# Kernel tuning notes

Hardware: AMD Instinct MI355X
Metric: run time of the kernel (lower is better)

The kernel has to match this reference:

```python
import jax, jax.numpy as jnp
import numpy as np
from jax import lax

B, S, H, A = 8, 2048, 16, 128   # batch, seq, num_head, i_head_dim
D = 128                          # o_head_dim
LN_EPS = 1e-6


def setup_inputs() -> dict:
    key = jax.random.key(0)
    ks = jax.random.split(key, 6)
    heads_input = jax.random.normal(ks[0], (B, S, H, A), dtype=jnp.float32)
    # grouped linear weights: (heads, in_per_head, out_per_head)
    w_hid = jax.random.normal(ks[1], (H, 2 * A, 3 * D), dtype=jnp.float32) * 0.02
    b_hid = jnp.zeros((H, 3 * D), dtype=jnp.float32)
    w_og = jax.random.normal(ks[2], (H, A + D, D), dtype=jnp.float32) * 0.02
    b_og = jnp.zeros((H, D), dtype=jnp.float32)
    ln_g = jnp.ones((H, A), dtype=jnp.float32)
    ln_b = jnp.zeros((H, A), dtype=jnp.float32)
    init_cx = jnp.zeros((H, D), dtype=jnp.float32)
    return {"heads_input": heads_input, "w_hid": w_hid, "b_hid": b_hid,
            "w_og": w_og, "b_og": b_og, "ln_g": ln_g, "ln_b": ln_b,
            "init_cx": init_cx}


def _ln2d(x, g, b):
    # LayerNorm over the last two dims (H, A)
    m = jnp.mean(x, axis=(-2, -1), keepdims=True)
    v = jnp.var(x, axis=(-2, -1), keepdims=True)
    return (x - m) * lax.rsqrt(v + LN_EPS) * g + b


def _forward(heads_input, w_hid, b_hid, w_og, b_og, ln_g, ln_b, init_cx):
    # cumulative-sum + LayerNorm (RS1cumsumstatnorm, states=None)
    csum = _ln2d(jnp.cumsum(heads_input, axis=1), ln_g, ln_b)  # (B,S,H,A)
    # grouped (per-head) linear: 2A -> 3D
    hid_in = jnp.concatenate([heads_input, csum], axis=-1)     # (B,S,H,2A)
    gates = jnp.einsum('bshi,hio->bsho', hid_in, w_hid) + b_hid  # (B,S,H,3D)
    igate, fgate, hidden = jnp.split(gates, 3, axis=-1)
    fgate = jax.nn.sigmoid(fgate)
    hidden = jax.nn.relu(hidden)
    igh = jax.nn.sigmoid(igate) * hidden                        # (B,S,H,D)
    # forget-gated linear recurrence c_t = f_t * c_{t-1} + igh_t (LGateFunc)
    def combine(c1, c2):
        a1, u1 = c1
        a2, u2 = c2
        return a1 * a2, u1 * a2 + u2
    F, C = lax.associative_scan(combine, (fgate, igh), axis=1)
    cell = C + F * init_cx[None, None]                          # (B,S,H,D)
    # output gate: grouped linear (A+D -> D), sigmoid, gate the cell
    og_in = jnp.concatenate([heads_input, cell], axis=-1)       # (B,S,H,A+D)
    og = jax.nn.sigmoid(jnp.einsum('bshi,hio->bsho', og_in, w_og) + b_og)
    return og * cell


def reference(heads_input, w_hid, b_hid, w_og, b_og, ln_g, ln_b, init_cx):
    return _forward(heads_input, w_hid, b_hid, w_og, b_og, ln_g, ln_b, init_cx)
```

## Files before the change

### kernel.cpp

```cpp
#include <hip/hip_runtime.h>
#include <stdint.h>

#define Bb 8
#define Ss 2048
#define Hh 16
#define Aa 128
#define Dd 128
#define NGATE 384
#define KDIM 256
#define NCH 16
#define CLEN 128
#define ROWS (Bb*Ss)
#define ROWSTR (Hh*Aa)

typedef float f32x4 __attribute__((ext_vector_type(4)));
typedef __bf16 bf16x8 __attribute__((ext_vector_type(8)));
typedef unsigned short u16x8 __attribute__((ext_vector_type(8)));

static __device__ __forceinline__ unsigned short f2bf(float f){
  unsigned int u = __builtin_bit_cast(unsigned int, f);
  u += 0x7FFFu + ((u >> 16) & 1u);
  return (unsigned short)(u >> 16);
}
static __device__ __forceinline__ float bf2f(unsigned short s){
  unsigned int u = ((unsigned int)s) << 16;
  return __builtin_bit_cast(float, u);
}
static __device__ __forceinline__ float sigf(float x){ return 1.0f/(1.0f + __expf(-x)); }

__global__ void k_conv_whid(const float* __restrict__ w, unsigned short* __restrict__ wt){
  int idx = blockIdx.x*256 + threadIdx.x;
  const int total = Hh*KDIM*NGATE;
  for (; idx < total; idx += gridDim.x*256){
    int o = idx % NGATE; int k = (idx/NGATE) % KDIM; int h = idx/(NGATE*KDIM);
    int g = o >> 7, d = o & 127;
    int nh = d >> 6, dl = d & 63;
    int wn = dl >> 4, ln15 = d & 15;
    int ks = k >> 5, lq = (k >> 3) & 3, kb = k & 7;
    int hy = h*2 + nh;
    int l = lq*16 + ln15;
    size_t dst = (size_t)hy*(192*KDIM) + (size_t)((((wn*8 + ks)*3 + g)*64 + l)*8 + kb);
    wt[dst] = f2bf(w[idx]);
  }
}
__global__ void k_conv_wog(const float* __restrict__ w, unsigned short* __restrict__ wt){
  int idx = blockIdx.x*256 + threadIdx.x;
  const int total = Hh*KDIM*Dd;
  for (; idx < total; idx += gridDim.x*256){
    int o = idx % Dd; int k = (idx/Dd) % KDIM; int h = idx/(Dd*KDIM);
    int wn = o >> 5, j = (o >> 4) & 1, ln15 = o & 15;
    int ks = k >> 5, lq = (k >> 3) & 3, kb = k & 7;
    int lane = lq*16 + ln15;
    size_t dst = (size_t)h*(Dd*KDIM) + (size_t)((((wn*8 + ks)*2 + j)*64 + lane)*8 + kb);
    wt[dst] = f2bf(w[idx]);
  }
}

__global__ void k_cumsum_a(const float* __restrict__ x, float* __restrict__ totals,
                           unsigned short* __restrict__ xbf){
  int c = blockIdx.x;
  int k = c % NCH; int hb = c / NCH;
  int b = hb / Hh, h = hb % Hh;
  int a = threadIdx.x;
  const size_t base = ((size_t)(b*Ss + k*CLEN)*Hh + h)*Aa + a;
  const float* p = x + base;
  unsigned short* xq = xbf + base;
  float run = 0.f;
  #pragma unroll 2
  for (int i = 0; i < CLEN; ++i){
    float v = p[(size_t)i*ROWSTR];
    run += v;
    xq[(size_t)i*ROWSTR] = f2bf(v);
  }
  totals[(size_t)c*Aa + a] = run;
}

__global__ void k_cumsum_c(const unsigned short* __restrict__ xbf, const float* __restrict__ totals,
                           unsigned short* __restrict__ csum){
  int c = blockIdx.x;
  int k = c % NCH; int hb = c / NCH;
  int b = hb / Hh, h = hb % Hh;
  int a = threadIdx.x;
  const float* tp = totals + (size_t)hb*NCH*Aa + a;
  float run = 0.f;
  for (int j = 0; j < k; ++j) run += tp[(size_t)j*Aa];
  const size_t base = ((size_t)(b*Ss + k*CLEN)*Hh + h)*Aa + a;
  const unsigned short* p = xbf + base;
  unsigned short* q = csum + base;
  #pragma unroll 2
  for (int i = 0; i < CLEN; ++i){
    run += bf2f(p[(size_t)i*ROWSTR]);
    q[(size_t)i*ROWSTR] = f2bf(run);
  }
}

__global__ void k_stats_ln(unsigned short* __restrict__ cs,
                           const float* __restrict__ ln_g, const float* __restrict__ ln_b){
  int r = blockIdx.x;
  int t = threadIdx.x;
  unsigned short* p = cs + (size_t)r*ROWSTR + t*8;
  u16x8 v = *(const u16x8*)p;
  float s = 0.f, q = 0.f;
  #pragma unroll
  for (int i = 0; i < 8; ++i){ float f = bf2f(v[i]); s += f; q += f*f; }
  #pragma unroll
  for (int off = 32; off; off >>= 1){ s += __shfl_down(s, off); q += __shfl_down(q, off); }
  __shared__ float ls[4], lq[4];
  __shared__ float2 mrs;
  int wid = t >> 6, lane = t & 63;
  if (lane == 0){ ls[wid] = s; lq[wid] = q; }
  __syncthreads();
  if (t == 0){
    float S2 = ls[0]+ls[1]+ls[2]+ls[3], Q = lq[0]+lq[1]+lq[2]+lq[3];
    float mu = S2 * (1.0f/(float)ROWSTR);
    float var = Q * (1.0f/(float)ROWSTR) - mu*mu;
    mrs = make_float2(mu, rsqrtf(var + 1e-6f));
  }
  __syncthreads();
  float mu = mrs.x, rstd = mrs.y;
  const float4* g4 = (const float4*)(ln_g + t*8);
  const float4* b4 = (const float4*)(ln_b + t*8);
  float4 g0 = g4[0], g1 = g4[1], b0 = b4[0], b1 = b4[1];
  u16x8 o;
  o[0] = f2bf((bf2f(v[0]) - mu)*rstd*g0.x + b0.x);
  o[1] = f2bf((bf2f(v[1]) - mu)*rstd*g0.y + b0.y);
  o[2] = f2bf((bf2f(v[2]) - mu)*rstd*g0.z + b0.z);
  o[3] = f2bf((bf2f(v[3]) - mu)*rstd*g0.w + b0.w);
  o[4] = f2bf((bf2f(v[4]) - mu)*rstd*g1.x + b1.x);
  o[5] = f2bf((bf2f(v[5]) - mu)*rstd*g1.y + b1.y);
  o[6] = f2bf((bf2f(v[6]) - mu)*rstd*g1.z + b1.z);
  o[7] = f2bf((bf2f(v[7]) - mu)*rstd*g1.w + b1.w);
  *(u16x8*)p = o;
}

#define GROWT(t_) ((mg*16 + (t_))*128)
__launch_bounds__(512, 2)
__global__ void k_gates(const unsigned short* __restrict__ xbf,
                        const unsigned short* __restrict__ csln,
                        const unsigned short* __restrict__ wht,
                        const float* __restrict__ b_hid, unsigned int* __restrict__ fu){
  __shared__ unsigned short lA[4][128*64];
  const int mg = blockIdx.x, hy = blockIdx.y;
  const int h = hy >> 1, nh = hy & 1;
  const int tid = threadIdx.x;
  const int lane = tid & 63, wid = tid >> 6;
  const int wm = wid & 1, wn = wid >> 1;
  const int ln15 = lane & 15, lq = lane >> 4;
  const int r0 = tid >> 3, q0 = tid & 7;
  const int lwA0 = (r0*128 + q0*16) ^ ((r0 & 7) << 4);
  const int lwA1 = ((r0+64)*128 + q0*16) ^ ((r0 & 7) << 4);

  bf16x8 Bf[8][3];
  {
    const u16x8* bs8 = (const u16x8*)(wht + (size_t)hy*(192*KDIM));
    #pragma unroll
    for (int ks = 0; ks < 8; ++ks)
      #pragma unroll
      for (int g = 0; g < 3; ++g)
        Bf[ks][g] = __builtin_bit_cast(bf16x8, bs8[((wn*8 + ks)*3 + g)*64 + lane]);
  }
  const int dcol = nh*64 + wn*16 + ln15;
  const float big = b_hid[h*NGATE + dcol];
  const float bfg = b_hid[h*NGATE + 128 + dcol];
  const float bhd = b_hid[h*NGATE + 256 + dcol];

  f32x4 acc[4][3];
  #pragma unroll
  for (int i = 0; i < 4; ++i)
    #pragma unroll
    for (int j = 0; j < 3; ++j) acc[i][j] = (f32x4){0.f,0.f,0.f,0.f};

  u16x8 pa0, pa1, pa2, pa3;

#define GA_FETCH(t_, half_) do { \
    const unsigned short* as_ = (half_) ? csln : xbf; \
    const size_t base_ = (size_t)(GROWT(t_) + r0)*ROWSTR + h*Aa + q0*8; \
    pa0 = *(const u16x8*)(as_ + base_); \
    pa1 = *(const u16x8*)(as_ + base_ + (size_t)64*ROWSTR); \
    pa2 = *(const u16x8*)(as_ + base_ + 64); \
    pa3 = *(const u16x8*)(as_ + base_ + 64 + (size_t)64*ROWSTR); \
  } while(0)
#define GA_WRITE(bp_) do { \
    *(u16x8*)((char*)lA[(bp_)*2+0] + lwA0) = pa0; \
    *(u16x8*)((char*)lA[(bp_)*2+0] + lwA1) = pa1; \
    *(u16x8*)((char*)lA[(bp_)*2+1] + lwA0) = pa2; \
    *(u16x8*)((char*)lA[(bp_)*2+1] + lwA1) = pa3; \
  } while(0)

  GA_FETCH(0, 0); GA_WRITE(0);
  GA_FETCH(0, 1);

  for (int t = 0; t < 16; ++t){
    #pragma unroll
    for (int half = 0; half < 2; ++half){
      __syncthreads();
      if (half == 0){
        GA_WRITE(1);
        GA_FETCH(t+1 < 16 ? t+1 : t, 0);
      } else if (t + 1 < 16){
        GA_WRITE(0);
        GA_FETCH(t+1, 1);
      }
      #pragma unroll
      for (int kk2 = 0; kk2 < 2; ++kk2){
        #pragma unroll
        for (int ks2 = 0; ks2 < 2; ++ks2){
          const int kel = ks2*32 + lq*8;
          bf16x8 af[4];
          #pragma unroll
          for (int mf = 0; mf < 4; ++mf){
            int ra = wm*64 + mf*16 + ln15;
            af[mf] = __builtin_bit_cast(bf16x8,
              *(const u16x8*)((const char*)lA[half*2 + kk2] + ((ra*128 + kel*2) ^ ((ra & 7) << 4))));
          }
          #pragma unroll
          for (int g = 0; g < 3; ++g)
            #pragma unroll
            for (int mf = 0; mf < 4; ++mf)
              acc[mf][g] = __builtin_amdgcn_mfma_f32_16x16x32_bf16(
                  af[mf], Bf[half*4 + kk2*2 + ks2][g], acc[mf][g], 0, 0, 0);
        }
      }
      if (half == 1){
        const int m0 = GROWT(t);
        #pragma unroll
        for (int mf = 0; mf < 4; ++mf){
          const int rowb = m0 + wm*64 + mf*16 + lq*4;
          f32x4 aig = acc[mf][0], afg = acc[mf][1], ahd = acc[mf][2];
          #pragma unroll
          for (int r = 0; r < 4; ++r){
            float fg = sigf(afg[r] + bfg);
            float uu = sigf(aig[r] + big) * fmaxf(ahd[r] + bhd, 0.0f);
            fu[(size_t)(rowb + r)*ROWSTR + h*Dd + dcol] =
              ((unsigned int)f2bf(uu) << 16) | (unsigned int)f2bf(fg);
          }
          acc[mf][0] = (f32x4){0.f,0.f,0.f,0.f};
          acc[mf][1] = (f32x4){0.f,0.f,0.f,0.f};
          acc[mf][2] = (f32x4){0.f,0.f,0.f,0.f};
        }
      }
    }
  }
#undef GA_FETCH
#undef GA_WRITE
}

__global__ void k_recur_a(const unsigned int* __restrict__ fu,
                          float* __restrict__ Fc, float* __restrict__ Cc){
  int c = blockIdx.x;
  int k = c % NCH; int hb = c / NCH;
  int b = hb / Hh, h = hb % Hh;
  int d = threadIdx.x;
  const unsigned int* p = fu + ((size_t)(b*Ss + k*CLEN)*Hh + h)*Dd + d;
  float F = 1.f, C = 0.f;
  #pragma unroll 4
  for (int i = 0; i < CLEN; ++i){
    unsigned int v = p[(size_t)i*ROWSTR];
    float f = bf2f((unsigned short)v);
    float u = bf2f((unsigned short)(v >> 16));
    C = fmaf(f, C, u);
    F *= f;
  }
  Fc[(size_t)c*Dd + d] = F;
  Cc[(size_t)c*Dd + d] = C;
}

__global__ void k_recur_b(const float* __restrict__ Fc, const float* __restrict__ Cc,
                          const float* __restrict__ init_cx, float* __restrict__ gcarry){
  int bh = blockIdx.x;
  int h = bh % Hh;
  int d = threadIdx.x;
  float carry = init_cx[h*Dd + d];
  for (int j = 0; j < NCH; ++j){
    size_t o = ((size_t)bh*NCH + j)*Dd + d;
    gcarry[o] = carry;
    carry = fmaf(Fc[o], carry, Cc[o]);
  }
}

#define CPITCH 132
#define XPITCH 136
__launch_bounds__(512, 4)
__global__ void k_og_fused(const unsigned short* __restrict__ xbf,
                           const unsigned int* __restrict__ fu,
                           const unsigned short* __restrict__ wog2,
                           const float* __restrict__ gcarry,
                           const float* __restrict__ b_og, float* __restrict__ out){
  __shared__ float s_cell[64*CPITCH];
  __shared__ unsigned short s_xa[64*XPITCH];
  __shared__ float2 s_scan[4*128];
  __shared__ float s_cc[128];
  const int mg = blockIdx.x;
  const int h  = blockIdx.y;
  const int tid = threadIdx.x;
  const int lane = tid & 63, wid = tid >> 6;
  const int wm = wid >> 2, wn = wid & 3;
  const int ln15 = lane & 15, lq = lane >> 4;
  const int rd = tid & 127, rq = tid >> 7;

  bf16x8 Bf[8][2];
  {
    const u16x8* bs8 = (const u16x8*)(wog2 + (size_t)h*(Dd*KDIM));
    #pragma unroll
    for (int ks = 0; ks < 8; ++ks)
      #pragma unroll
      for (int j = 0; j < 2; ++j)
        Bf[ks][j] = __builtin_bit_cast(bf16x8, bs8[((wn*8 + ks)*2 + j)*64 + lane]);
  }
  if (tid < 128)
    s_cc[tid] = gcarry[((size_t)((mg>>2)*Hh + h)*NCH + (mg & 3)*4)*Dd + tid];
  __syncthreads();

  f32x4 acc[2][2];
  #pragma unroll
  for (int i = 0; i < 2; ++i){ acc[i][0] = (f32x4){0,0,0,0}; acc[i][1] = (f32x4){0,0,0,0}; }

  for (int t = 0; t < 8; ++t){
    const int row0 = mg*512 + t*64;
    unsigned int uf[16];
    const unsigned int* fp = fu + (size_t)(row0 + rq*16)*ROWSTR + h*Dd + rd;
    #pragma unroll
    for (int i = 0; i < 16; ++i) uf[i] = fp[(size_t)i*ROWSTR];
    #pragma unroll
    for (int i = 0; i < 2; ++i){
      int c = tid + i*512;
      int r = c >> 4, c8 = c & 15;
      *(u16x8*)&s_xa[r*XPITCH + c8*8] =
        *(const u16x8*)(xbf + (size_t)(row0 + r)*ROWSTR + h*Aa + c8*8);
    }
    float F = 1.f, C = 0.f;
    #pragma unroll
    for (int i = 0; i < 16; ++i){
      float f = bf2f((unsigned short)uf[i]);
      float u = bf2f((unsigned short)(uf[i] >> 16));
      C = fmaf(f, C, u); F *= f;
    }
    s_scan[rq*128 + rd] = make_float2(F, C);
    __syncthreads();
    float cin = s_cc[rd];
    #pragma unroll
    for (int qq = 0; qq < 3; ++qq){
      if (rq > qq){ float2 s = s_scan[qq*128 + rd]; cin = fmaf(s.x, cin, s.y); }
    }
    __syncthreads();
    if (rq == 3){ float2 s3 = s_scan[3*128 + rd]; s_cc[rd] = fmaf(s3.x, cin, s3.y); }
    {
      float c = cin;
      #pragma unroll
      for (int i = 0; i < 16; ++i){
        float f = bf2f((unsigned short)uf[i]);
        float u = bf2f((unsigned short)(uf[i] >> 16));
        c = fmaf(f, c, u);
        s_cell[(rq*16 + i)*CPITCH + rd] = c;
      }
    }
    __syncthreads();
    #pragma unroll
    for (int ks = 0; ks < 4; ++ks){
      bf16x8 af[2];
      #pragma unroll
      for (int mf = 0; mf < 2; ++mf){
        int ra = wm*32 + mf*16 + ln15;
        af[mf] = __builtin_bit_cast(bf16x8,
          *(const u16x8*)&s_xa[ra*XPITCH + ks*32 + lq*8]);
      }
      #pragma unroll
      for (int mf = 0; mf < 2; ++mf)
        #pragma unroll
        for (int j = 0; j < 2; ++j)
          acc[mf][j] = __builtin_amdgcn_mfma_f32_16x16x32_bf16(af[mf], Bf[ks][j], acc[mf][j], 0, 0, 0);
    }
    #pragma unroll
    for (int ks = 4; ks < 8; ++ks){
      bf16x8 af[2];
      #pragma unroll
      for (int mf = 0; mf < 2; ++mf){
        int ra = wm*32 + mf*16 + ln15;
        const float* cp = &s_cell[ra*CPITCH + (ks-4)*32 + lq*8];
        f32x4 c0 = *(const f32x4*)cp;
        f32x4 c1 = *(const f32x4*)(cp + 4);
        u16x8 tt;
        tt[0]=f2bf(c0[0]); tt[1]=f2bf(c0[1]); tt[2]=f2bf(c0[2]); tt[3]=f2bf(c0[3]);
        tt[4]=f2bf(c1[0]); tt[5]=f2bf(c1[1]); tt[6]=f2bf(c1[2]); tt[7]=f2bf(c1[3]);
        af[mf] = __builtin_bit_cast(bf16x8, tt);
      }
      #pragma unroll
      for (int mf = 0; mf < 2; ++mf)
        #pragma unroll
        for (int j = 0; j < 2; ++j)
          acc[mf][j] = __builtin_amdgcn_mfma_f32_16x16x32_bf16(af[mf], Bf[ks][j], acc[mf][j], 0, 0, 0);
    }
    #pragma unroll
    for (int mf = 0; mf < 2; ++mf){
      const int rl = wm*32 + mf*16 + lq*4;
      #pragma unroll
      for (int j = 0; j < 2; ++j){
        const int d = wn*32 + j*16 + ln15;
        const float bo = b_og[h*Dd + d];
        #pragma unroll
        for (int r = 0; r < 4; ++r){
          float cell = s_cell[(rl + r)*CPITCH + d];
          out[(size_t)(row0 + rl + r)*ROWSTR + h*Dd + d] = sigf(acc[mf][j][r] + bo) * cell;
        }
        acc[mf][j] = (f32x4){0.f,0.f,0.f,0.f};
      }
    }
    __syncthreads();
  }
}

extern "C" void kernel_launch(void* const* d_in, const int* in_sizes, int n_in,
                              void* d_out, int out_size, void* d_ws, size_t ws_size,
                              hipStream_t stream){
  const float* x       = (const float*)d_in[0];
  const float* w_hid   = (const float*)d_in[1];
  const float* b_hid   = (const float*)d_in[2];
  const float* w_og    = (const float*)d_in[3];
  const float* b_og    = (const float*)d_in[4];
  const float* ln_g    = (const float*)d_in[5];
  const float* ln_b    = (const float*)d_in[6];
  const float* init_cx = (const float*)d_in[7];
  float* out = (float*)d_out;

  char* ws = (char*)d_ws;
  unsigned short* csum = (unsigned short*)(ws);
  unsigned int*   fu   = (unsigned int*)  (ws + ((size_t)64  << 20));
  unsigned short* xbf  = (unsigned short*)(ws + ((size_t)192 << 20));
  float*          tot  = (float*)         (ws + ((size_t)256 << 20));
  float*          Fc   = (float*)         (ws + ((size_t)257 << 20));
  float*          Cc   = (float*)         (ws + ((size_t)258 << 20));
  unsigned short* wht  = (unsigned short*)(ws + ((size_t)260 << 20));
  unsigned short* wot  = (unsigned short*)(ws + ((size_t)263 << 20));
  float*          gcar = (float*)         (ws + ((size_t)264 << 20));

  k_conv_whid<<<2048, 256, 0, stream>>>(w_hid, wht);
  k_conv_wog <<<1024, 256, 0, stream>>>(w_og,  wot);
  k_cumsum_a <<<Bb*Hh*NCH, Aa, 0, stream>>>(x, tot, xbf);
  k_cumsum_c <<<Bb*Hh*NCH, Aa, 0, stream>>>(xbf, tot, csum);
  k_stats_ln <<<ROWS, 256, 0, stream>>>(csum, ln_g, ln_b);
  k_gates    <<<dim3(8, 32), 512, 0, stream>>>(xbf, csum, wht, b_hid, fu);
  k_recur_a  <<<Bb*Hh*NCH, Dd, 0, stream>>>(fu, Fc, Cc);
  k_recur_b  <<<Bb*Hh, Dd, 0, stream>>>(Fc, Cc, init_cx, gcar);
  k_og_fused <<<dim3(32, 16), 512, 0, stream>>>(xbf, fu, wot, gcar, b_og, out);
}
```

Baseline: 310.7 us.

## Shrink gates kernel register and LDS footprint to double occupancy and grid

The gates GEMM kernel no longer keeps all 24 weight fragments resident in registers. It reloads half of them (12 fragments) from global memory twice per row tile, and the LDS A buffer is halved to a 2-stage 64-wide K pipeline. Launch bounds rise to 4 blocks per CU, and the grid doubles to 512 blocks with 8 row tiles each, to improve occupancy and latency hiding on 256 CUs. In exchange, weight fragments are re-fetched from global/L2 every tile and there are more barriers per tile.

New measurement: 425.1 us. 36.8% more time.

```diff
diff --git a/kernel.cpp b/kernel.cpp
--- a/kernel.cpp
+++ b/kernel.cpp
@@ -133,13 +133,13 @@
   *(u16x8*)p = o;
 }
 
-#define GROWT(t_) ((mg*16 + (t_))*128)
-__launch_bounds__(512, 2)
+#define GROWT(t_) ((mg*8 + (t_))*128)
+__launch_bounds__(512, 4)
 __global__ void k_gates(const unsigned short* __restrict__ xbf,
                         const unsigned short* __restrict__ csln,
                         const unsigned short* __restrict__ wht,
                         const float* __restrict__ b_hid, unsigned int* __restrict__ fu){
-  __shared__ unsigned short lA[4][128*64];
+  __shared__ unsigned short lA[2][128*64];
   const int mg = blockIdx.x, hy = blockIdx.y;
   const int h = hy >> 1, nh = hy & 1;
   const int tid = threadIdx.x;
@@ -149,79 +149,77 @@
   const int r0 = tid >> 3, q0 = tid & 7;
   const int lwA0 = (r0*128 + q0*16) ^ ((r0 & 7) << 4);
   const int lwA1 = ((r0+64)*128 + q0*16) ^ ((r0 & 7) << 4);
-
-  bf16x8 Bf[8][3];
-  {
-    const u16x8* bs8 = (const u16x8*)(wht + (size_t)hy*(192*KDIM));
-    #pragma unroll
-    for (int ks = 0; ks < 8; ++ks)
-      #pragma unroll
-      for (int g = 0; g < 3; ++g)
-        Bf[ks][g] = __builtin_bit_cast(bf16x8, bs8[((wn*8 + ks)*3 + g)*64 + lane]);
-  }
+  const u16x8* bs8 = (const u16x8*)(wht + (size_t)hy*(192*KDIM));
+
   const int dcol = nh*64 + wn*16 + ln15;
   const float big = b_hid[h*NGATE + dcol];
   const float bfg = b_hid[h*NGATE + 128 + dcol];
   const float bhd = b_hid[h*NGATE + 256 + dcol];
 
+  bf16x8 Bf[4][3];
   f32x4 acc[4][3];
   #pragma unroll
   for (int i = 0; i < 4; ++i)
     #pragma unroll
     for (int j = 0; j < 3; ++j) acc[i][j] = (f32x4){0.f,0.f,0.f,0.f};
 
-  u16x8 pa0, pa1, pa2, pa3;
-
-#define GA_FETCH(t_, half_) do { \
-    const unsigned short* as_ = (half_) ? csln : xbf; \
-    const size_t base_ = (size_t)(GROWT(t_) + r0)*ROWSTR + h*Aa + q0*8; \
+  u16x8 pa0, pa1;
+
+#define GB_LOAD(half_) do { \
+    _Pragma("unroll") \
+    for (int sl_ = 0; sl_ < 4; ++sl_) \
+      _Pragma("unroll") \
+      for (int g_ = 0; g_ < 3; ++g_) \
+        Bf[sl_][g_] = __builtin_bit_cast(bf16x8, \
+          bs8[((wn*8 + (half_)*4 + sl_)*3 + g_)*64 + lane]); \
+  } while(0)
+#define GA_FETCH(t_, kk_) do { \
+    const unsigned short* as_ = ((kk_) < 2) ? xbf : csln; \
+    const size_t base_ = (size_t)(GROWT(t_) + r0)*ROWSTR + h*Aa + ((kk_) & 1)*64 + q0*8; \
     pa0 = *(const u16x8*)(as_ + base_); \
     pa1 = *(const u16x8*)(as_ + base_ + (size_t)64*ROWSTR); \
-    pa2 = *(const u16x8*)(as_ + base_ + 64); \
-    pa3 = *(const u16x8*)(as_ + base_ + 64 + (size_t)64*ROWSTR); \
   } while(0)
-#define GA_WRITE(bp_) do { \
-    *(u16x8*)((char*)lA[(bp_)*2+0] + lwA0) = pa0; \
-    *(u16x8*)((char*)lA[(bp_)*2+0] + lwA1) = pa1; \
-    *(u16x8*)((char*)lA[(bp_)*2+1] + lwA0) = pa2; \
-    *(u16x8*)((char*)lA[(bp_)*2+1] + lwA1) = pa3; \
+#define GA_WRITE(buf_) do { \
+    *(u16x8*)((char*)lA[buf_] + lwA0) = pa0; \
+    *(u16x8*)((char*)lA[buf_] + lwA1) = pa1; \
   } while(0)
 
   GA_FETCH(0, 0); GA_WRITE(0);
   GA_FETCH(0, 1);
 
-  for (int t = 0; t < 16; ++t){
-    #pragma unroll
-    for (int half = 0; half < 2; ++half){
+  for (int t = 0; t < 8; ++t){
+    #pragma unroll
+    for (int kk = 0; kk < 4; ++kk){
+      const int cur = kk & 1;
       __syncthreads();
-      if (half == 0){
-        GA_WRITE(1);
-        GA_FETCH(t+1 < 16 ? t+1 : t, 0);
-      } else if (t + 1 < 16){
-        GA_WRITE(0);
+      if (kk == 0) GB_LOAD(0);
+      if (kk == 2) GB_LOAD(1);
+      if (kk < 3){
+        GA_WRITE(cur^1);
+        if (kk + 2 < 4) GA_FETCH(t, kk+2);
+        else if (t + 1 < 8) GA_FETCH(t+1, 0);
+      } else if (t + 1 < 8){
+        GA_WRITE(cur^1);
         GA_FETCH(t+1, 1);
       }
       #pragma unroll
-      for (int kk2 = 0; kk2 < 2; ++kk2){
-        #pragma unroll
-        for (int ks2 = 0; ks2 < 2; ++ks2){
-          const int kel = ks2*32 + lq*8;
-          bf16x8 af[4];
+      for (int ks2 = 0; ks2 < 2; ++ks2){
+        const int kel = ks2*32 + lq*8;
+        bf16x8 af[4];
+        #pragma unroll
+        for (int mf = 0; mf < 4; ++mf){
+          int ra = wm*64 + mf*16 + ln15;
+          af[mf] = __builtin_bit_cast(bf16x8,
+            *(const u16x8*)((const char*)lA[cur] + ((ra*128 + kel*2) ^ ((ra & 7) << 4))));
+        }
+        #pragma unroll
+        for (int g = 0; g < 3; ++g)
           #pragma unroll
-          for (int mf = 0; mf < 4; ++mf){
-            int ra = wm*64 + mf*16 + ln15;
-            af[mf] = __builtin_bit_cast(bf16x8,
-              *(const u16x8*)((const char*)lA[half*2 + kk2] + ((ra*128 + kel*2) ^ ((ra & 7) << 4))));
-          }
-          #pragma unroll
-          for (int g = 0; g < 3; ++g)
-            #pragma unroll
-            for (int mf = 0; mf < 4; ++mf)
-              acc[mf][g] = __builtin_amdgcn_mfma_f32_16x16x32_bf16(
-                  af[mf], Bf[half*4 + kk2*2 + ks2][g], acc[mf][g], 0, 0, 0);
-        }
-      }
-      if (half == 1){
+          for (int mf = 0; mf < 4; ++mf)
+            acc[mf][g] = __builtin_amdgcn_mfma_f32_16x16x32_bf16(
+                af[mf], Bf[(kk & 1)*2 + ks2][g], acc[mf][g], 0, 0, 0);
+      }
+      if (kk == 3){
         const int m0 = GROWT(t);
         #pragma unroll
         for (int mf = 0; mf < 4; ++mf){
@@ -241,6 +239,7 @@
       }
     }
   }
+#undef GB_LOAD
 #undef GA_FETCH
 #undef GA_WRITE
 }
@@ -438,7 +437,7 @@
   k_cumsum_a <<<Bb*Hh*NCH, Aa, 0, stream>>>(x, tot, xbf);
   k_cumsum_c <<<Bb*Hh*NCH, Aa, 0, stream>>>(xbf, tot, csum);
   k_stats_ln <<<ROWS, 256, 0, stream>>>(csum, ln_g, ln_b);
-  k_gates    <<<dim3(8, 32), 512, 0, stream>>>(xbf, csum, wht, b_hid, fu);
+  k_gates    <<<dim3(16, 32), 512, 0, stream>>>(xbf, csum, wht, b_hid, fu);
   k_recur_a  <<<Bb*Hh*NCH, Dd, 0, stream>>>(fu, Fc, Cc);
   k_recur_b  <<<Bb*Hh, Dd, 0, stream>>>(Fc, Cc, init_cx, gcar);
   k_og_fused <<<dim3(32, 16), 512, 0, stream>>>(xbf, fu, wot, gcar, b_og, out);
```
